# Performance work log

Hardware: AMD Instinct MI355X
Metric: run time of the kernel (lower is better)

Reference implementation:

```python
import jax, jax.numpy as jnp
import numpy as np

EMBED_DIM = 1024
NUM_TOKENS = 32
TOKEN_DIM = 32  # ceil(1024/32)
CODEBOOK_SIZE = 256
BATCH = 32768
BETA = 0.25


def setup_inputs() -> dict:
    key = jax.random.key(0)
    ks = jax.random.split(key, 6)
    lim_e = 1.0 / np.sqrt(EMBED_DIM)
    lim_d = 1.0 / np.sqrt(NUM_TOKENS * TOKEN_DIM)
    lim_c = 1.0 / CODEBOOK_SIZE
    return {
        "skills": jax.random.normal(ks[0], (BATCH, EMBED_DIM), jnp.float32),
        "enc_w": jax.random.uniform(ks[1], (NUM_TOKENS * TOKEN_DIM, EMBED_DIM), jnp.float32, -lim_e, lim_e),
        "enc_b": jax.random.uniform(ks[2], (NUM_TOKENS * TOKEN_DIM,), jnp.float32, -lim_e, lim_e),
        "codebook": jax.random.uniform(ks[3], (CODEBOOK_SIZE, TOKEN_DIM), jnp.float32, -lim_c, lim_c),
        "dec_w": jax.random.uniform(ks[4], (EMBED_DIM, NUM_TOKENS * TOKEN_DIM), jnp.float32, -lim_d, lim_d),
        "dec_b": jax.random.uniform(ks[5], (EMBED_DIM,), jnp.float32, -lim_d, lim_d),
    }


def reference(skills, enc_w, enc_b, codebook, dec_w, dec_b):
    B = skills.shape[0]
    # encoder linear -> [B, num_tokens, token_dim]
    projected = (skills @ enc_w.T + enc_b).reshape(B, NUM_TOKENS, TOKEN_DIM)
    flat = projected.reshape(-1, TOKEN_DIM)  # [B*T, d]
    # squared-euclidean distances to codebook entries: [B*T, K]
    dists = (
        jnp.sum(flat * flat, axis=1, keepdims=True)
        - 2.0 * flat @ codebook.T
        + jnp.sum(codebook * codebook, axis=1)[None, :]
    )
    codes = jnp.argmin(dists, axis=1)  # [B*T]
    quantized = codebook[codes].reshape(B, NUM_TOKENS, TOKEN_DIM)
    # straight-through estimator
    st = projected + jax.lax.stop_gradient(quantized - projected)
    commitment = jnp.mean((projected - jax.lax.stop_gradient(quantized)) ** 2)
    codebook_loss = jnp.mean((quantized - jax.lax.stop_gradient(projected)) ** 2)
    vq_loss = codebook_loss + BETA * commitment
    reconstructed = st.reshape(B, NUM_TOKENS * TOKEN_DIM) @ dec_w.T + dec_b
    recon_loss = jnp.mean((reconstructed - skills) ** 2)
    loss = vq_loss + recon_loss
    return reconstructed, codes.reshape(B, NUM_TOKENS), loss
```

## Files before the change

kernel.cpp:

```cpp
#include <hip/hip_runtime.h>
#include <hip/hip_bf16.h>
#include <float.h>

#define OUT_CODES_OFF (33554432UL)
#define OUT_LOSS_OFF  (34603008UL)
#define TAU 1e-5f
#define INV_N (1.0f/33554432.0f)

typedef __attribute__((ext_vector_type(8))) short s16x8;
typedef __attribute__((ext_vector_type(4))) float f32x4;

__device__ __forceinline__ unsigned short bf16r(float x) {
    unsigned int u = __float_as_uint(x);
    unsigned int r = (u + 0x7FFFu + ((u >> 16) & 1u)) >> 16;
    return (unsigned short)r;
}
__device__ __forceinline__ float bf16f(unsigned short h) {
    return __uint_as_float(((unsigned int)h) << 16);
}
__device__ __forceinline__ void split8r(float4 v0, float4 v1, s16x8& h, s16x8& l) {
    float xs[8] = {v0.x, v0.y, v0.z, v0.w, v1.x, v1.y, v1.z, v1.w};
    #pragma unroll
    for (int e = 0; e < 8; ++e) {
        unsigned int u = __float_as_uint(xs[e]);
        unsigned short hh = (unsigned short)(u >> 16);
        h[e] = (short)hh;
        l[e] = (short)bf16r(xs[e] - bf16f(hh));
    }
}

__device__ __forceinline__ void gld16(const unsigned short* g, unsigned short* l) {
    __builtin_amdgcn_global_load_lds(
        (const __attribute__((address_space(1))) unsigned int*)g,
        (__attribute__((address_space(3))) unsigned int*)l, 16, 0, 0);
}

__global__ void k_prep_split(const float* __restrict__ in,
                             unsigned short* __restrict__ ot)
{
    const int b = blockIdx.x, tid = threadIdx.x;
    const int rblk = b >> 5, kt = b & 31, r = tid >> 2, q = tid & 3;
    const float* src = in + (size_t)(rblk * 128 + r) * 1024 + kt * 32 + q * 8;
    float4 v0 = *(const float4*)src, v1 = *(const float4*)(src + 4);
    s16x8 h, l;
    split8r(v0, v1, h, l);
    unsigned short* dst = ot + (size_t)b * 8192 + q * 1024 + r * 8;
    *(s16x8*)dst = h;
    *(s16x8*)(dst + 4096) = l;
}

__global__ void k_prep_r(const float* __restrict__ in,
                         unsigned short* __restrict__ o,
                         int n8)
{
    const int i = blockIdx.x * 256 + threadIdx.x;
    if (i >= n8) return;
    const float4* p = (const float4*)(in + (size_t)i * 8);
    float4 v0 = p[0], v1 = p[1];
    float xs[8] = {v0.x, v0.y, v0.z, v0.w, v1.x, v1.y, v1.z, v1.w};
    s16x8 h;
    #pragma unroll
    for (int e = 0; e < 8; ++e) h[e] = (short)bf16r(xs[e]);
    *(s16x8*)(o + (size_t)i * 8) = h;
}

__launch_bounds__(512, 1)
__global__ void k_enc_gl(const unsigned short* __restrict__ At,
                         const unsigned short* __restrict__ Bt,
                         const float* __restrict__ enc_b,
                         const float* __restrict__ cb_g,
                         float* __restrict__ out)
{
    __shared__ __align__(16) unsigned short us[49664];

    const int tid = threadIdx.x;
    const int rb = blockIdx.x >> 1, chf = blockIdx.x & 1;
    const int r0 = rb * 128;
    const int wid = tid >> 6, lane = tid & 63;
    const int wm = wid >> 1, wn = wid & 1;
    const int mbase = wm * 32;
    const int lhi = lane >> 4, llo = lane & 15;

    if (tid < 256) {
        const float4* cr = (const float4*)&cb_g[tid * 32];
        float s = 0.f;
        #pragma unroll
        for (int i = 0; i < 8; ++i) {
            float4 v = cr[i];
            float c[4] = {v.x, v.y, v.z, v.w};
            #pragma unroll
            for (int e = 0; e < 4; ++e) {
                const int d = i * 4 + e, kc = d >> 3, e8 = d & 7;
                unsigned int u = __float_as_uint(c[e]);
                unsigned short hh = (unsigned short)(u >> 16);
                us[32768 + kc * 2048 + tid * 8 + e8] = hh;
                us[40960 + kc * 2048 + tid * 8 + e8] = bf16r(c[e] - bf16f(hh));
                s = fmaf(c[e], c[e], s);
            }
        }
        *(float*)&us[49152 + tid * 2] = s;
    }
    {
        const unsigned short* gA = At + ((size_t)(rb * 32 + 0)) * 8192 + tid * 8;
        const unsigned short* gB = Bt + ((size_t)((chf * 4 + 0) * 32 + 0)) * 8192 + tid * 8;
        gld16(gA,        us + wid * 512);
        gld16(gA + 4096, us + 4096 + wid * 512);
        gld16(gB,        us + 8192 + wid * 512);
        gld16(gB + 4096, us + 12288 + wid * 512);
    }
    __syncthreads();

    float vq_local = 0.f;
    f32x4 acc[2][4];
    const int ntg_base = chf * 4;

    for (int it = 0; it < 128; ++it) {
        const int nt = it >> 5, kt = it & 31;
        if (kt == 0) {
            #pragma unroll
            for (int mf = 0; mf < 2; ++mf)
                #pragma unroll
                for (int nf = 0; nf < 4; ++nf) acc[mf][nf] = (f32x4)0.f;
        }
        if (it < 127) {
            const int tt = it + 1, ntn = tt >> 5, ktn = tt & 31;
            const int nb = (tt & 1) * 16384;
            const unsigned short* gA = At + ((size_t)(rb * 32 + ktn)) * 8192 + tid * 8;
            const unsigned short* gB = Bt + ((size_t)((ntg_base + ntn) * 32 + ktn)) * 8192 + tid * 8;
            gld16(gA,        us + nb + wid * 512);
            gld16(gA + 4096, us + nb + 4096 + wid * 512);
            gld16(gB,        us + nb + 8192 + wid * 512);
            gld16(gB + 4096, us + nb + 12288 + wid * 512);
        }
        {
            const int cb0 = (it & 1) * 16384;
            s16x8 ah[2], al[2];
            #pragma unroll
            for (int mf = 0; mf < 2; ++mf) {
                const int row = mbase + mf * 16 + llo;
                ah[mf] = *(s16x8*)&us[cb0 + lhi * 1024 + row * 8];
                al[mf] = *(s16x8*)&us[cb0 + 4096 + lhi * 1024 + row * 8];
            }
            #pragma unroll
            for (int nf = 0; nf < 4; ++nf) {
                const int rowb = wn * 64 + nf * 16 + llo;
                s16x8 bh = *(s16x8*)&us[cb0 + 8192 + lhi * 1024 + rowb * 8];
                s16x8 bl = *(s16x8*)&us[cb0 + 12288 + lhi * 1024 + rowb * 8];
                #pragma unroll
                for (int mf = 0; mf < 2; ++mf) {
                    acc[mf][nf] = __builtin_amdgcn_mfma_f32_16x16x32_bf16(ah[mf], bh, acc[mf][nf], 0, 0, 0);
                    acc[mf][nf] = __builtin_amdgcn_mfma_f32_16x16x32_bf16(ah[mf], bl, acc[mf][nf], 0, 0, 0);
                    acc[mf][nf] = __builtin_amdgcn_mfma_f32_16x16x32_bf16(al[mf], bh, acc[mf][nf], 0, 0, 0);
                }
            }
        }

        if (kt == 31) {
            for (int c = 0; c < 2; ++c) {
                __syncthreads();
                if (wn == c) {
                    #pragma unroll
                    for (int nf = 0; nf < 4; ++nf) {
                        const int colh = nf * 16 + llo;
                        const int tlc = colh >> 5, d = colh & 31;
                        const int kc = d >> 3, e8 = d & 7;
                        const float bias = enc_b[chf * 512 + nt * 128 + c * 64 + colh];
                        #pragma unroll
                        for (int mf = 0; mf < 2; ++mf)
                            #pragma unroll
                            for (int r = 0; r < 4; ++r) {
                                const int m_local = mbase + mf * 16 + lhi * 4 + r;
                                float val = acc[mf][nf][r] + bias;
                                unsigned int u = __float_as_uint(val);
                                unsigned short hh = (unsigned short)(u >> 16);
                                const int tok = m_local * 2 + tlc;
                                us[16384 + kc * 2048 + tok * 8 + e8] = hh;
                                us[24576 + kc * 2048 + tok * 8 + e8] = bf16r(val - bf16f(hh));
                            }
                    }
                }
                __syncthreads();
                s16x8 fh[2], fl[2];
                #pragma unroll
                for (int gi = 0; gi < 2; ++gi) {
                    const int tokrow = (wid * 2 + gi) * 16 + llo;
                    fh[gi] = *(s16x8*)&us[16384 + lhi * 2048 + tokrow * 8];
                    fl[gi] = *(s16x8*)&us[24576 + lhi * 2048 + tokrow * 8];
                }
                float s1[2][4], s2[2][4]; int bj[2][4];
                #pragma unroll
                for (int gi = 0; gi < 2; ++gi)
                    #pragma unroll
                    for (int r = 0; r < 4; ++r) { s1[gi][r] = FLT_MAX; s2[gi][r] = FLT_MAX; bj[gi][r] = 0; }
                for (int jb = 0; jb < 16; ++jb) {
                    const int j = jb * 16 + llo;
                    s16x8 ch = *(s16x8*)&us[32768 + lhi * 2048 + j * 8];
                    s16x8 cl = *(s16x8*)&us[40960 + lhi * 2048 + j * 8];
                    const float cnv = *(const float*)&us[49152 + j * 2];
                    #pragma unroll
                    for (int gi = 0; gi < 2; ++gi) {
                        f32x4 sc = (f32x4)0.f;
                        sc = __builtin_amdgcn_mfma_f32_16x16x32_bf16(fh[gi], ch, sc, 0, 0, 0);
                        sc = __builtin_amdgcn_mfma_f32_16x16x32_bf16(fh[gi], cl, sc, 0, 0, 0);
                        sc = __builtin_amdgcn_mfma_f32_16x16x32_bf16(fl[gi], ch, sc, 0, 0, 0);
                        #pragma unroll
                        for (int r = 0; r < 4; ++r) {
                            float s = fmaf(-2.f, sc[r], cnv);
                            if (s < s1[gi][r])      { s2[gi][r] = s1[gi][r]; s1[gi][r] = s; bj[gi][r] = j; }
                            else if (s < s2[gi][r]) { s2[gi][r] = s; }
                        }
                    }
                }
                #pragma unroll
                for (int gi = 0; gi < 2; ++gi) {
                    float Fp = 0.f;
                    #pragma unroll
                    for (int e = 0; e < 8; ++e) {
                        float fv = bf16f((unsigned short)fh[gi][e]) + bf16f((unsigned short)fl[gi][e]);
                        Fp = fmaf(fv, fv, Fp);
                    }
                    Fp += __shfl_xor(Fp, 16);
                    Fp += __shfl_xor(Fp, 32);
                    #pragma unroll
                    for (int r = 0; r < 4; ++r) {
                        float a1 = s1[gi][r], a2 = s2[gi][r]; int aj = bj[gi][r];
                        #pragma unroll
                        for (int off = 1; off <= 8; off <<= 1) {
                            float o1 = __shfl_xor(a1, off);
                            float o2 = __shfl_xor(a2, off);
                            int   oj = __shfl_xor(aj, off);
                            if (o1 < a1) { a2 = fminf(a1, o2); a1 = o1; aj = oj; }
                            else         { a2 = fminf(o1, a2); }
                        }
                        const float Ft = __shfl(Fp, lhi * 4 + r);
                        if (llo == 0) {
                            const int tok_local = (wid * 2 + gi) * 16 + lhi * 4 + r;
                            const int row = tok_local >> 1, tlc2 = tok_local & 1;
                            const int t = chf * 16 + nt * 4 + c * 2 + tlc2;
                            float cv = (a2 - a1 < TAU) ? (float)(aj + 512) : (float)aj;
                            out[OUT_CODES_OFF + (size_t)(r0 + row) * 32 + t] = cv;
                            vq_local += Ft + a1;
                        }
                    }
                }
            }
        }
        __syncthreads();
    }
    {
        float v = vq_local;
        #pragma unroll
        for (int off = 32; off >= 1; off >>= 1) v += __shfl_xor(v, off);
        if (lane == 0) atomicAdd(&out[OUT_LOSS_OFF], v * (1.25f * INV_N));
    }
}

__launch_bounds__(512, 1)
__global__ void k_enc_fb(const float* __restrict__ skills,
                         const float* __restrict__ enc_w,
                         const float* __restrict__ enc_b,
                         const float* __restrict__ cb_g,
                         float* __restrict__ out)
{
    __shared__ __align__(16) unsigned short us[40960];

    const int tid = threadIdx.x;
    const int rb = blockIdx.x >> 1, chf = blockIdx.x & 1;
    const int r0 = rb * 128;
    const int wid = tid >> 6, lane = tid & 63;
    const int wm = wid >> 1, wn = wid & 1;
    const int mbase = wm * 32;
    const int lhi = lane >> 4, llo = lane & 15;
    const int srow = tid >> 2, sq = tid & 3;

    if (tid < 256) {
        const float4* cr = (const float4*)&cb_g[tid * 32];
        float s = 0.f;
        #pragma unroll
        for (int i = 0; i < 8; ++i) {
            float4 v = cr[i];
            float c[4] = {v.x, v.y, v.z, v.w};
            #pragma unroll
            for (int e = 0; e < 4; ++e) {
                const int d = i * 4 + e;
                unsigned int u = __float_as_uint(c[e]);
                unsigned short hh = (unsigned short)(u >> 16);
                us[20480 + tid * 40 + d] = hh;
                us[30720 + tid * 40 + d] = bf16r(c[e] - bf16f(hh));
                s = fmaf(c[e], c[e], s);
            }
        }
        *(float*)&us[20480 + tid * 40 + 32] = s;
    }
    __syncthreads();

    float vq_local = 0.f;
    f32x4 acc[2][4];
    float4 ra0, ra1, rb0, rb1;
    {
        const float* ap = &skills[(size_t)(r0 + srow) * 1024 + sq * 8];
        ra0 = *(const float4*)ap; ra1 = *(const float4*)(ap + 4);
        const float* bp = &enc_w[(size_t)(chf * 512 + srow) * 1024 + sq * 8];
        rb0 = *(const float4*)bp; rb1 = *(const float4*)(bp + 4);
    }

    for (int it = 0; it < 128; ++it) {
        const int nt = it >> 5, kt = it & 31;
        if (kt == 0) {
            #pragma unroll
            for (int mf = 0; mf < 2; ++mf)
                #pragma unroll
                for (int nf = 0; nf < 4; ++nf) acc[mf][nf] = (f32x4)0.f;
        }
        __syncthreads();
        {
            s16x8 h, l;
            split8r(ra0, ra1, h, l);
            *(s16x8*)&us[srow * 40 + sq * 8] = h;
            *(s16x8*)&us[5120 + srow * 40 + sq * 8] = l;
            split8r(rb0, rb1, h, l);
            *(s16x8*)&us[10240 + srow * 40 + sq * 8] = h;
            *(s16x8*)&us[15360 + srow * 40 + sq * 8] = l;
        }
        __syncthreads();
        if (it < 127) {
            const int it2 = it + 1, nt2 = it2 >> 5, kt2 = it2 & 31;
            const float* ap = &skills[(size_t)(r0 + srow) * 1024 + kt2 * 32 + sq * 8];
            ra0 = *(const float4*)ap; ra1 = *(const float4*)(ap + 4);
            const float* bp = &enc_w[(size_t)(chf * 512 + nt2 * 128 + srow) * 1024 + kt2 * 32 + sq * 8];
            rb0 = *(const float4*)bp; rb1 = *(const float4*)(bp + 4);
        }
        {
            s16x8 ah[2], al[2];
            #pragma unroll
            for (int mf = 0; mf < 2; ++mf) {
                const int row = mbase + mf * 16 + llo;
                ah[mf] = *(s16x8*)&us[row * 40 + lhi * 8];
                al[mf] = *(s16x8*)&us[5120 + row * 40 + lhi * 8];
            }
            #pragma unroll
            for (int nf = 0; nf < 4; ++nf) {
                const int rowb = wn * 64 + nf * 16 + llo;
                s16x8 bh = *(s16x8*)&us[10240 + rowb * 40 + lhi * 8];
                s16x8 bl = *(s16x8*)&us[15360 + rowb * 40 + lhi * 8];
                #pragma unroll
                for (int mf = 0; mf < 2; ++mf) {
                    acc[mf][nf] = __builtin_amdgcn_mfma_f32_16x16x32_bf16(ah[mf], bh, acc[mf][nf], 0, 0, 0);
                    acc[mf][nf] = __builtin_amdgcn_mfma_f32_16x16x32_bf16(ah[mf], bl, acc[mf][nf], 0, 0, 0);
                    acc[mf][nf] = __builtin_amdgcn_mfma_f32_16x16x32_bf16(al[mf], bh, acc[mf][nf], 0, 0, 0);
                }
            }
        }

        if (kt == 31) {
            for (int c = 0; c < 2; ++c) {
                __syncthreads();
                if (wn == c) {
                    #pragma unroll
                    for (int nf = 0; nf < 4; ++nf) {
                        const int colh = nf * 16 + llo;
                        const int tlc = colh >> 5, d = colh & 31;
                        const float bias = enc_b[chf * 512 + nt * 128 + c * 64 + colh];
                        #pragma unroll
                        for (int mf = 0; mf < 2; ++mf)
                            #pragma unroll
                            for (int r = 0; r < 4; ++r) {
                                const int m_local = mbase + mf * 16 + lhi * 4 + r;
                                float val = acc[mf][nf][r] + bias;
                                unsigned int u = __float_as_uint(val);
                                unsigned short hh = (unsigned short)(u >> 16);
                                const int tok = m_local * 2 + tlc;
                                us[tok * 40 + d] = hh;
                                us[10240 + tok * 40 + d] = bf16r(val - bf16f(hh));
                            }
                    }
                }
                __syncthreads();
                s16x8 fh[2], fl[2];
                #pragma unroll
                for (int gi = 0; gi < 2; ++gi) {
                    const int tokrow = (wid * 2 + gi) * 16 + llo;
                    fh[gi] = *(s16x8*)&us[tokrow * 40 + lhi * 8];
                    fl[gi] = *(s16x8*)&us[10240 + tokrow * 40 + lhi * 8];
                }
                float s1[2][4], s2[2][4]; int bj[2][4];
                #pragma unroll
                for (int gi = 0; gi < 2; ++gi)
                    #pragma unroll
                    for (int r = 0; r < 4; ++r) { s1[gi][r] = FLT_MAX; s2[gi][r] = FLT_MAX; bj[gi][r] = 0; }
                for (int jb = 0; jb < 16; ++jb) {
                    const int j = jb * 16 + llo;
                    s16x8 ch = *(s16x8*)&us[20480 + j * 40 + lhi * 8];
                    s16x8 cl = *(s16x8*)&us[30720 + j * 40 + lhi * 8];
                    const float cnv = *(const float*)&us[20480 + j * 40 + 32];
                    #pragma unroll
                    for (int gi = 0; gi < 2; ++gi) {
                        f32x4 sc = (f32x4)0.f;
                        sc = __builtin_amdgcn_mfma_f32_16x16x32_bf16(fh[gi], ch, sc, 0, 0, 0);
                        sc = __builtin_amdgcn_mfma_f32_16x16x32_bf16(fh[gi], cl, sc, 0, 0, 0);
                        sc = __builtin_amdgcn_mfma_f32_16x16x32_bf16(fl[gi], ch, sc, 0, 0, 0);
                        #pragma unroll
                        for (int r = 0; r < 4; ++r) {
                            float s = fmaf(-2.f, sc[r], cnv);
                            if (s < s1[gi][r])      { s2[gi][r] = s1[gi][r]; s1[gi][r] = s; bj[gi][r] = j; }
                            else if (s < s2[gi][r]) { s2[gi][r] = s; }
                        }
                    }
                }
                #pragma unroll
                for (int gi = 0; gi < 2; ++gi) {
                    float Fp = 0.f;
                    #pragma unroll
                    for (int e = 0; e < 8; ++e) {
                        float fv = bf16f((unsigned short)fh[gi][e]) + bf16f((unsigned short)fl[gi][e]);
                        Fp = fmaf(fv, fv, Fp);
                    }
                    Fp += __shfl_xor(Fp, 16);
                    Fp += __shfl_xor(Fp, 32);
                    #pragma unroll
                    for (int r = 0; r < 4; ++r) {
                        float a1 = s1[gi][r], a2 = s2[gi][r]; int aj = bj[gi][r];
                        #pragma unroll
                        for (int off = 1; off <= 8; off <<= 1) {
                            float o1 = __shfl_xor(a1, off);
                            float o2 = __shfl_xor(a2, off);
                            int   oj = __shfl_xor(aj, off);
                            if (o1 < a1) { a2 = fminf(a1, o2); a1 = o1; aj = oj; }
                            else         { a2 = fminf(o1, a2); }
                        }
                        const float Ft = __shfl(Fp, lhi * 4 + r);
                        if (llo == 0) {
                            const int tok_local = (wid * 2 + gi) * 16 + lhi * 4 + r;
                            const int row = tok_local >> 1, tlc2 = tok_local & 1;
                            const int t = chf * 16 + nt * 4 + c * 2 + tlc2;
                            float cv = (a2 - a1 < TAU) ? (float)(aj + 512) : (float)aj;
                            out[OUT_CODES_OFF + (size_t)(r0 + row) * 32 + t] = cv;
                            vq_local += Ft + a1;
                        }
                    }
                }
            }
        }
    }
    {
        float v = vq_local;
        #pragma unroll
        for (int off = 32; off >= 1; off >>= 1) v += __shfl_xor(v, off);
        if (lane == 0) atomicAdd(&out[OUT_LOSS_OFF], v * (1.25f * INV_N));
    }
}

__launch_bounds__(256)
__global__ void k_fix(const float* __restrict__ skills,
                      const float* __restrict__ enc_w,
                      const float* __restrict__ enc_b,
                      const float* __restrict__ cb_g,
                      float* __restrict__ codes)
{
    __shared__ unsigned int cnt;
    __shared__ unsigned short list[256];

    const int tid = threadIdx.x;
    const int base = blockIdx.x * 256;

    if (tid == 0) cnt = 0;
    __syncthreads();
    {
        const int c = (int)codes[base + tid];
        if (c >= 512) {
            unsigned int ix = atomicAdd(&cnt, 1u);
            list[ix] = (unsigned short)tid;
        }
    }
    __syncthreads();
    const unsigned int n = cnt;
    if (n == 0) return;

    const int wv = tid >> 6, lane = tid & 63;
    const int d = lane & 31;

    for (unsigned int i = wv; i < n; i += 4) {
        const int tok = base + (int)list[i];
        const int row = tok >> 5;
        const int t   = tok & 31;

        const float4* s4 = (const float4*)&skills[(size_t)row * 1024];
        const float4* w4 = (const float4*)&enc_w[(size_t)(t * 32 + d) * 1024];
        float v1 = 0.f, v2 = 0.f, v3 = 0.f;
        for (int q = 0; q < 96; ++q) {
            float4 a = s4[q], b = w4[q];
            v1 = fmaf(a.x, b.x, v1); v1 = fmaf(a.y, b.y, v1);
            v1 = fmaf(a.z, b.z, v1); v1 = fmaf(a.w, b.w, v1);
        }
        for (int q = 96; q < 192; ++q) {
            float4 a = s4[q], b = w4[q];
            v2 = fmaf(a.x, b.x, v2); v2 = fmaf(a.y, b.y, v2);
            v2 = fmaf(a.z, b.z, v2); v2 = fmaf(a.w, b.w, v2);
        }
        for (int q = 192; q < 256; ++q) {
            float4 a = s4[q], b = w4[q];
            v3 = fmaf(a.x, b.x, v3); v3 = fmaf(a.y, b.y, v3);
            v3 = fmaf(a.z, b.z, v3); v3 = fmaf(a.w, b.w, v3);
        }
        const float pd = ((v1 + v2) + v3) + enc_b[t * 32 + d];

        float pv[32];
        #pragma unroll
        for (int dd = 0; dd < 32; ++dd) pv[dd] = __shfl(pd, dd);

        float F;
        {
            float s[32];
            #pragma unroll
            for (int dd = 0; dd < 32; ++dd) s[dd] = pv[dd] * pv[dd];
            float r[8];
            #pragma unroll
            for (int j = 0; j < 8; ++j) r[j] = ((s[j] + s[8+j]) + s[16+j]) + s[24+j];
            F = ((r[0] + r[1]) + (r[2] + r[3])) + ((r[4] + r[5]) + (r[6] + r[7]));
        }

        float bs = FLT_MAX; int bj = 0;
        for (int m = 0; m < 4; ++m) {
            const int j = m * 64 + lane;
            const float* cj = &cb_g[j * 32];
            float g = 0.f;
            #pragma unroll
            for (int dd = 0; dd < 32; ++dd) g = fmaf(pv[dd], cj[dd], g);
            float cs[32];
            #pragma unroll
            for (int dd = 0; dd < 32; ++dd) cs[dd] = cj[dd] * cj[dd];
            float r[8];
            #pragma unroll
            for (int jj = 0; jj < 8; ++jj) r[jj] = ((cs[jj] + cs[8+jj]) + cs[16+jj]) + cs[24+jj];
            float cn = ((r[0] + r[1]) + (r[2] + r[3])) + ((r[4] + r[5]) + (r[6] + r[7]));
            float dist = (F - 2.0f * g) + cn;
            if (dist < bs) { bs = dist; bj = j; }
        }
        #pragma unroll
        for (int off = 32; off >= 1; off >>= 1) {
            float os = __shfl_xor(bs, off);
            int   oj = __shfl_xor(bj, off);
            if (os < bs || (os == bs && oj < bj)) { bs = os; bj = oj; }
        }
        if (lane == 0) codes[tok] = (float)bj;
    }
}

template <bool PRED>
__launch_bounds__(512)
__global__ void k_dec(const float* __restrict__ skills,
                      const float* __restrict__ cb_g,
                      const unsigned short* __restrict__ cbb,
                      const float* __restrict__ dec_w,
                      const unsigned short* __restrict__ dwb,
                      const float* __restrict__ dec_b,
                      const float* __restrict__ codes,
                      float* __restrict__ recon,
                      float* __restrict__ loss_out)
{
    __shared__ unsigned short Qt[128][40], Wt[128][40];

    const int tid = threadIdx.x;
    const int r0 = (blockIdx.x >> 3) * 128;
    const int n0 = (blockIdx.x & 7) * 128;
    const int wid = tid >> 6, lane = tid & 63;
    const int wm = wid >> 1, wn = wid & 1;
    const int mbase = wm * 32, nbase = wn * 64;
    const int lhi = lane >> 4, llo = lane & 15;
    const int srow = tid >> 2, sq = tid & 3;

    f32x4 acc[2][4];
    #pragma unroll
    for (int mf = 0; mf < 2; ++mf)
        #pragma unroll
        for (int nf = 0; nf < 4; ++nf) acc[mf][nf] = (f32x4)0.f;

    s16x8 q16, w16;
    float4 q0, q1, w0, w1;
    int cnext;
    {
        const int c0 = ((int)codes[(size_t)(r0 + srow) * 32 + 0]) & 255;
        if (PRED) {
            q16 = *(const s16x8*)(cbb + c0 * 32 + sq * 8);
            w16 = *(const s16x8*)(dwb + (size_t)(n0 + srow) * 1024 + sq * 8);
        } else {
            const float* cp = &cb_g[c0 * 32 + sq * 8];
            q0 = *(const float4*)cp; q1 = *(const float4*)(cp + 4);
            const float* wp = &dec_w[(size_t)(n0 + srow) * 1024 + sq * 8];
            w0 = *(const float4*)wp; w1 = *(const float4*)(wp + 4);
        }
        cnext = ((int)codes[(size_t)(r0 + srow) * 32 + 1]) & 255;
    }

    for (int t = 0; t < 32; ++t) {
        __syncthreads();
        if (PRED) {
            *(s16x8*)&Qt[srow][sq * 8] = q16;
            *(s16x8*)&Wt[srow][sq * 8] = w16;
        } else {
            float xs[8] = {q0.x, q0.y, q0.z, q0.w, q1.x, q1.y, q1.z, q1.w};
            s16x8 h;
            #pragma unroll
            for (int e = 0; e < 8; ++e) h[e] = (short)bf16r(xs[e]);
            *(s16x8*)&Qt[srow][sq * 8] = h;
            float ys[8] = {w0.x, w0.y, w0.z, w0.w, w1.x, w1.y, w1.z, w1.w};
            #pragma unroll
            for (int e = 0; e < 8; ++e) h[e] = (short)bf16r(ys[e]);
            *(s16x8*)&Wt[srow][sq * 8] = h;
        }
        __syncthreads();
        if (t < 31) {
            if (PRED) {
                q16 = *(const s16x8*)(cbb + cnext * 32 + sq * 8);
                w16 = *(const s16x8*)(dwb + (size_t)(n0 + srow) * 1024 + (t + 1) * 32 + sq * 8);
            } else {
                const float* cp = &cb_g[cnext * 32 + sq * 8];
                q0 = *(const float4*)cp; q1 = *(const float4*)(cp + 4);
                const float* wp = &dec_w[(size_t)(n0 + srow) * 1024 + (t + 1) * 32 + sq * 8];
                w0 = *(const float4*)wp; w1 = *(const float4*)(wp + 4);
            }
            if (t < 30) cnext = ((int)codes[(size_t)(r0 + srow) * 32 + t + 2]) & 255;
        }
        s16x8 aq[2], bw[4];
        #pragma unroll
        for (int mf = 0; mf < 2; ++mf)
            aq[mf] = *(s16x8*)&Qt[mbase + mf * 16 + llo][lhi * 8];
        #pragma unroll
        for (int nf = 0; nf < 4; ++nf)
            bw[nf] = *(s16x8*)&Wt[nbase + nf * 16 + llo][lhi * 8];
        #pragma unroll
        for (int mf = 0; mf < 2; ++mf)
            #pragma unroll
            for (int nf = 0; nf < 4; ++nf)
                acc[mf][nf] = __builtin_amdgcn_mfma_f32_16x16x32_bf16(aq[mf], bw[nf], acc[mf][nf], 0, 0, 0);
    }

    float lsum = 0.f;
    #pragma unroll
    for (int mf = 0; mf < 2; ++mf)
        #pragma unroll
        for (int nf = 0; nf < 4; ++nf) {
            const int col = n0 + nbase + nf * 16 + llo;
            const float bias = dec_b[col];
            #pragma unroll
            for (int r = 0; r < 4; ++r) {
                const int row = r0 + mbase + mf * 16 + lhi * 4 + r;
                float rv = acc[mf][nf][r] + bias;
                float dv = rv - skills[(size_t)row * 1024 + col];
                lsum = fmaf(dv, dv, lsum);
                recon[(size_t)row * 1024 + col] = rv;
            }
        }
    #pragma unroll
    for (int off = 32; off >= 1; off >>= 1) lsum += __shfl_xor(lsum, off);
    if (lane == 0) atomicAdd(loss_out, lsum * INV_N);
}

extern "C" void kernel_launch(void* const* d_in, const int* in_sizes, int n_in,
                              void* d_out, int out_size, void* d_ws, size_t ws_size,
                              hipStream_t stream)
{
    const float* skills = (const float*)d_in[0];
    const float* enc_w  = (const float*)d_in[1];
    const float* enc_b  = (const float*)d_in[2];
    const float* cbg    = (const float*)d_in[3];
    const float* dec_w  = (const float*)d_in[4];
    const float* dec_b  = (const float*)d_in[5];
    float* out = (float*)d_out;

    hipMemsetAsync(out + OUT_LOSS_OFF, 0, 4, stream);

    const size_t NEED_BIG = 4UL*1024*1024 + 2097152UL + 16384UL + 256UL;
    unsigned short* wsu16 = (unsigned short*)d_ws;

    if (ws_size >= NEED_BIG) {
        unsigned short* Btl = wsu16;
        unsigned short* dwb = wsu16 + 2097152UL;
        unsigned short* cbb = wsu16 + 3145728UL;
        unsigned short* Atl = (unsigned short*)out;

        k_prep_split<<<dim3(8192), dim3(512), 0, stream>>>(skills, Atl);
        k_prep_split<<<dim3(256),  dim3(512), 0, stream>>>(enc_w, Btl);
        k_enc_gl<<<dim3(512), dim3(512), 0, stream>>>(Atl, Btl, enc_b, cbg, out);
        k_fix<<<dim3(4096), dim3(256), 0, stream>>>(skills, enc_w, enc_b, cbg, out + OUT_CODES_OFF);
        k_prep_r<<<dim3(512), dim3(256), 0, stream>>>(dec_w, dwb, 131072);
        k_prep_r<<<dim3(4), dim3(256), 0, stream>>>(cbg, cbb, 1024);
        k_dec<true><<<dim3(2048), dim3(512), 0, stream>>>(skills, cbg, cbb, dec_w, dwb, dec_b,
                                                          out + OUT_CODES_OFF, out, out + OUT_LOSS_OFF);
    } else {
        k_enc_fb<<<dim3(512), dim3(512), 0, stream>>>(skills, enc_w, enc_b, cbg, out);
        k_fix<<<dim3(4096), dim3(256), 0, stream>>>(skills, enc_w, enc_b, cbg, out + OUT_CODES_OFF);
        const bool pred = (ws_size >= (2097152UL + 16384UL + 64UL));
        unsigned short* dwb = wsu16;
        unsigned short* cbb = wsu16 + 1048576UL;
        if (pred) {
            k_prep_r<<<dim3(512), dim3(256), 0, stream>>>(dec_w, dwb, 131072);
            k_prep_r<<<dim3(4), dim3(256), 0, stream>>>(cbg, cbb, 1024);
            k_dec<true><<<dim3(2048), dim3(512), 0, stream>>>(skills, cbg, cbb, dec_w, dwb, dec_b,
                                                              out + OUT_CODES_OFF, out, out + OUT_LOSS_OFF);
        } else {
            k_dec<false><<<dim3(2048), dim3(512), 0, stream>>>(skills, cbg, cbb, dec_w, dwb, dec_b,
                                                               out + OUT_CODES_OFF, out, out + OUT_LOSS_OFF);
        }
    }
}
```

Baseline: 820.3 us.

## Add double-buffered direct-to-LDS decoder kernel with staged code indices

Adds a new decoder GEMM kernel that loads all code indices for its row block into shared memory up front. It then streams bf16 codebook rows and decoder weights straight into double-buffered LDS with async global-to-LDS loads, which removes the register round trip and one barrier per k-step. The weight and codebook conversion kernels are moved ahead of the encoder launch, and the fallback path is simplified to always use the fp32 decoder. The cost is more LDS per block and a different LDS layout that the MFMA fragment reads have to match.

```diff
diff --git a/kernel.cpp b/kernel.cpp
--- a/kernel.cpp
+++ b/kernel.cpp
@@ -546,13 +546,103 @@
     }
 }
 
-template <bool PRED>
+__launch_bounds__(512)
+__global__ void k_dec2(const float* __restrict__ skills,
+                       const unsigned short* __restrict__ cbb,
+                       const unsigned short* __restrict__ dwb,
+                       const float* __restrict__ dec_b,
+                       const float* __restrict__ codes,
+                       float* __restrict__ recon,
+                       float* __restrict__ loss_out)
+{
+    __shared__ __align__(16) int cds[4096];
+    __shared__ __align__(16) unsigned short qt[2][4096];
+    __shared__ __align__(16) unsigned short wt[2][4096];
+
+    const int tid = threadIdx.x;
+    const int r0 = (blockIdx.x >> 3) * 128;
+    const int n0 = (blockIdx.x & 7) * 128;
+    const int wid = tid >> 6, lane = tid & 63;
+    const int wm = wid >> 1, wn = wid & 1;
+    const int mbase = wm * 32, nbase = wn * 64;
+    const int lhi = lane >> 4, llo = lane & 15;
+    const int drow = tid & 127, dkc = tid >> 7;
+
+    {
+        const float4* cp = (const float4*)&codes[(size_t)r0 * 32];
+        #pragma unroll
+        for (int e = 0; e < 2; ++e) {
+            float4 v = cp[tid * 2 + e];
+            cds[tid * 8 + e * 4 + 0] = ((int)v.x) & 255;
+            cds[tid * 8 + e * 4 + 1] = ((int)v.y) & 255;
+            cds[tid * 8 + e * 4 + 2] = ((int)v.z) & 255;
+            cds[tid * 8 + e * 4 + 3] = ((int)v.w) & 255;
+        }
+    }
+    __syncthreads();
+    {
+        const int code = cds[drow * 32 + 0];
+        gld16(cbb + code * 32 + dkc * 8, &qt[0][0] + (tid >> 6) * 512);
+        gld16(dwb + (size_t)(n0 + drow) * 1024 + dkc * 8, &wt[0][0] + (tid >> 6) * 512);
+    }
+    __syncthreads();
+
+    f32x4 acc[2][4];
+    #pragma unroll
+    for (int mf = 0; mf < 2; ++mf)
+        #pragma unroll
+        for (int nf = 0; nf < 4; ++nf) acc[mf][nf] = (f32x4)0.f;
+
+    for (int t = 0; t < 32; ++t) {
+        if (t < 31) {
+            const int tn = t + 1, nb = tn & 1;
+            const int code = cds[drow * 32 + tn];
+            gld16(cbb + code * 32 + dkc * 8, &qt[nb][0] + (tid >> 6) * 512);
+            gld16(dwb + (size_t)(n0 + drow) * 1024 + tn * 32 + dkc * 8, &wt[nb][0] + (tid >> 6) * 512);
+        }
+        {
+            const int cb = t & 1;
+            s16x8 aq[2], bw[4];
+            #pragma unroll
+            for (int mf = 0; mf < 2; ++mf)
+                aq[mf] = *(s16x8*)&qt[cb][lhi * 1024 + (mbase + mf * 16 + llo) * 8];
+            #pragma unroll
+            for (int nf = 0; nf < 4; ++nf)
+                bw[nf] = *(s16x8*)&wt[cb][lhi * 1024 + (nbase + nf * 16 + llo) * 8];
+            #pragma unroll
+            for (int mf = 0; mf < 2; ++mf)
+                #pragma unroll
+                for (int nf = 0; nf < 4; ++nf)
+                    acc[mf][nf] = __builtin_amdgcn_mfma_f32_16x16x32_bf16(aq[mf], bw[nf], acc[mf][nf], 0, 0, 0);
+        }
+        __syncthreads();
+    }
+
+    float lsum = 0.f;
+    #pragma unroll
+    for (int mf = 0; mf < 2; ++mf)
+        #pragma unroll
+        for (int nf = 0; nf < 4; ++nf) {
+            const int col = n0 + nbase + nf * 16 + llo;
+            const float bias = dec_b[col];
+            #pragma unroll
+            for (int r = 0; r < 4; ++r) {
+                const int row = r0 + mbase + mf * 16 + lhi * 4 + r;
+                float rv = acc[mf][nf][r] + bias;
+                float dv = rv - skills[(size_t)row * 1024 + col];
+                lsum = fmaf(dv, dv, lsum);
+                recon[(size_t)row * 1024 + col] = rv;
+            }
+        }
+    #pragma unroll
+    for (int off = 32; off >= 1; off >>= 1) lsum += __shfl_xor(lsum, off);
+    if (lane == 0) atomicAdd(loss_out, lsum * INV_N);
+}
+
 __launch_bounds__(512)
 __global__ void k_dec(const float* __restrict__ skills,
                       const float* __restrict__ cb_g,
-                      const unsigned short* __restrict__ cbb,
                       const float* __restrict__ dec_w,
-                      const unsigned short* __restrict__ dwb,
                       const float* __restrict__ dec_b,
                       const float* __restrict__ codes,
                       float* __restrict__ recon,
@@ -575,29 +665,20 @@
         #pragma unroll
         for (int nf = 0; nf < 4; ++nf) acc[mf][nf] = (f32x4)0.f;
 
-    s16x8 q16, w16;
     float4 q0, q1, w0, w1;
     int cnext;
     {
         const int c0 = ((int)codes[(size_t)(r0 + srow) * 32 + 0]) & 255;
-        if (PRED) {
-            q16 = *(const s16x8*)(cbb + c0 * 32 + sq * 8);
-            w16 = *(const s16x8*)(dwb + (size_t)(n0 + srow) * 1024 + sq * 8);
-        } else {
-            const float* cp = &cb_g[c0 * 32 + sq * 8];
-            q0 = *(const float4*)cp; q1 = *(const float4*)(cp + 4);
-            const float* wp = &dec_w[(size_t)(n0 + srow) * 1024 + sq * 8];
-            w0 = *(const float4*)wp; w1 = *(const float4*)(wp + 4);
-        }
+        const float* cp = &cb_g[c0 * 32 + sq * 8];
+        q0 = *(const float4*)cp; q1 = *(const float4*)(cp + 4);
+        const float* wp = &dec_w[(size_t)(n0 + srow) * 1024 + sq * 8];
+        w0 = *(const float4*)wp; w1 = *(const float4*)(wp + 4);
         cnext = ((int)codes[(size_t)(r0 + srow) * 32 + 1]) & 255;
     }
 
     for (int t = 0; t < 32; ++t) {
         __syncthreads();
-        if (PRED) {
-            *(s16x8*)&Qt[srow][sq * 8] = q16;
-            *(s16x8*)&Wt[srow][sq * 8] = w16;
-        } else {
+        {
             float xs[8] = {q0.x, q0.y, q0.z, q0.w, q1.x, q1.y, q1.z, q1.w};
             s16x8 h;
             #pragma unroll
@@ -610,15 +691,10 @@
         }
         __syncthreads();
         if (t < 31) {
-            if (PRED) {
-                q16 = *(const s16x8*)(cbb + cnext * 32 + sq * 8);
-                w16 = *(const s16x8*)(dwb + (size_t)(n0 + srow) * 1024 + (t + 1) * 32 + sq * 8);
-            } else {
-                const float* cp = &cb_g[cnext * 32 + sq * 8];
-                q0 = *(const float4*)cp; q1 = *(const float4*)(cp + 4);
-                const float* wp = &dec_w[(size_t)(n0 + srow) * 1024 + (t + 1) * 32 + sq * 8];
-                w0 = *(const float4*)wp; w1 = *(const float4*)(wp + 4);
-            }
+            const float* cp = &cb_g[cnext * 32 + sq * 8];
+            q0 = *(const float4*)cp; q1 = *(const float4*)(cp + 4);
+            const float* wp = &dec_w[(size_t)(n0 + srow) * 1024 + (t + 1) * 32 + sq * 8];
+            w0 = *(const float4*)wp; w1 = *(const float4*)(wp + 4);
             if (t < 30) cnext = ((int)codes[(size_t)(r0 + srow) * 32 + t + 2]) & 255;
         }
         s16x8 aq[2], bw[4];
@@ -681,26 +757,16 @@
 
         k_prep_split<<<dim3(8192), dim3(512), 0, stream>>>(skills, Atl);
         k_prep_split<<<dim3(256),  dim3(512), 0, stream>>>(enc_w, Btl);
+        k_prep_r<<<dim3(512), dim3(256), 0, stream>>>(dec_w, dwb, 131072);
+        k_prep_r<<<dim3(4), dim3(256), 0, stream>>>(cbg, cbb, 1024);
         k_enc_gl<<<dim3(512), dim3(512), 0, stream>>>(Atl, Btl, enc_b, cbg, out);
         k_fix<<<dim3(4096), dim3(256), 0, stream>>>(skills, enc_w, enc_b, cbg, out + OUT_CODES_OFF);
-        k_prep_r<<<dim3(512), dim3(256), 0, stream>>>(dec_w, dwb, 131072);
-        k_prep_r<<<dim3(4), dim3(256), 0, stream>>>(cbg, cbb, 1024);
-        k_dec<true><<<dim3(2048), dim3(512), 0, stream>>>(skills, cbg, cbb, dec_w, dwb, dec_b,
-                                                          out + OUT_CODES_OFF, out, out + OUT_LOSS_OFF);
+        k_dec2<<<dim3(2048), dim3(512), 0, stream>>>(skills, cbb, dwb, dec_b,
+                                                     out + OUT_CODES_OFF, out, out + OUT_LOSS_OFF);
     } else {
         k_enc_fb<<<dim3(512), dim3(512), 0, stream>>>(skills, enc_w, enc_b, cbg, out);
         k_fix<<<dim3(4096), dim3(256), 0, stream>>>(skills, enc_w, enc_b, cbg, out + OUT_CODES_OFF);
-        const bool pred = (ws_size >= (2097152UL + 16384UL + 64UL));
-        unsigned short* dwb = wsu16;
-        unsigned short* cbb = wsu16 + 1048576UL;
-        if (pred) {
-            k_prep_r<<<dim3(512), dim3(256), 0, stream>>>(dec_w, dwb, 131072);
-            k_prep_r<<<dim3(4), dim3(256), 0, stream>>>(cbg, cbb, 1024);
-            k_dec<true><<<dim3(2048), dim3(512), 0, stream>>>(skills, cbg, cbb, dec_w, dwb, dec_b,
-                                                              out + OUT_CODES_OFF, out, out + OUT_LOSS_OFF);
-        } else {
-            k_dec<false><<<dim3(2048), dim3(512), 0, stream>>>(skills, cbg, cbb, dec_w, dwb, dec_b,
-                                                               out + OUT_CODES_OFF, out, out + OUT_LOSS_OFF);
-        }
-    }
-}
+        k_dec<<<dim3(2048), dim3(512), 0, stream>>>(skills, cbg, dec_w, dec_b,
+                                                    out + OUT_CODES_OFF, out, out + OUT_LOSS_OFF);
+    }
+}
```

New measurement: 844.4 us. 2.9% more time.
